# Performance work log

Hardware: AMD Instinct MI355X
Metric: run time of the kernel (lower is better)

The kernel has to match this reference:

```python
import jax, jax.numpy as jnp
import numpy as np

B, T, I, E, H = 512, 1024, 32, 32, 256  # batch, seq, input, time-enc, hidden


def setup_inputs() -> dict:
    key = jax.random.key(0)
    ks = jax.random.split(key, 10)
    s = 0.05
    return {
        "X": jax.random.normal(ks[0], (B, T, I), dtype=jnp.float32),
        "encoded_timestamps": jax.random.normal(ks[1], (B, T, E), dtype=jnp.float32),
        "mask": jax.random.randint(ks[2], (B, T), 0, 2).astype(bool),
        # GRU layer 0: input = I + E
        "w_ih0": jax.random.normal(ks[3], (3 * H, I + E), dtype=jnp.float32) * s,
        "w_hh0": jax.random.normal(ks[4], (3 * H, H), dtype=jnp.float32) * s,
        "b_ih0": jnp.zeros((3 * H,), jnp.float32),
        "b_hh0": jnp.zeros((3 * H,), jnp.float32),
        # GRU layer 1: input = H
        "w_ih1": jax.random.normal(ks[5], (3 * H, H), dtype=jnp.float32) * s,
        "w_hh1": jax.random.normal(ks[6], (3 * H, H), dtype=jnp.float32) * s,
        "b_ih1": jnp.zeros((3 * H,), jnp.float32),
        "b_hh1": jnp.zeros((3 * H,), jnp.float32),
        # readout Linear(H -> I)
        "w_out": jax.random.normal(ks[7], (I, H), dtype=jnp.float32) * s,
        "b_out": jnp.zeros((I,), jnp.float32),
    }


def _gru_cell(x, h, w_ih, w_hh, b_ih, b_hh):
    # torch GRU cell semantics (gate order r, z, n)
    gi = x @ w_ih.T + b_ih
    gh = h @ w_hh.T + b_hh
    i_r, i_z, i_n = jnp.split(gi, 3, axis=-1)
    h_r, h_z, h_n = jnp.split(gh, 3, axis=-1)
    r = jax.nn.sigmoid(i_r + h_r)
    z = jax.nn.sigmoid(i_z + h_z)
    n = jnp.tanh(i_n + r * h_n)
    return (1.0 - z) * n + z * h


def reference(X, encoded_timestamps, mask,
              w_ih0, w_hh0, b_ih0, b_hh0,
              w_ih1, w_hh1, b_ih1, b_hh1,
              w_out, b_out):
    b, t, _ = X.shape
    hdim = w_hh0.shape[1]
    tm1 = t - 1

    def step(carry, xs):
        h0, h1, y = carry
        x_t, e_t, m_t, first = xs          # x_t [B,I], e_t [B,E], m_t [B], first scalar bool
        keep = m_t | first
        inp = jnp.concatenate([jnp.where(keep[:, None], x_t, y), e_t], axis=-1)
        h0 = _gru_cell(inp, h0, w_ih0, w_hh0, b_ih0, b_hh0)
        h1 = _gru_cell(h0, h1, w_ih1, w_hh1, b_ih1, b_hh1)
        y = h1 @ w_out.T + b_out
        return (h0, h1, y), y

    init = (jnp.zeros((b, hdim), X.dtype),
            jnp.zeros((b, hdim), X.dtype),
            jnp.zeros((b, X.shape[2]), X.dtype))
    xs = (jnp.swapaxes(X[:, :tm1], 0, 1),
          jnp.swapaxes(encoded_timestamps[:, 1:], 0, 1),
          jnp.swapaxes(mask[:, :tm1], 0, 1),
          jnp.arange(tm1) == 0)
    (h0, h1, _), outs = jax.lax.scan(step, init, xs)
    output_sequence = jnp.swapaxes(outs, 0, 1)  # [B, T-1, I]
    return output_sequence, h1  # h1 == h_t[-1]
```

## Files before the change

kernel.cpp:

```cpp
#include <hip/hip_runtime.h>
#include <stdint.h>
#include <stddef.h>

typedef unsigned short u16;
typedef unsigned int u32;
typedef unsigned long long u64;
typedef __attribute__((ext_vector_type(8))) short short8;
typedef __attribute__((ext_vector_type(4))) float f32x4;
typedef __attribute__((ext_vector_type(2))) float f32x2;

#define B_    512
#define T_    1024
#define TM1_  1023
#define I_    32
#define E_    32
#define H_    256
#define GSZ   8
#define NGRP  32
#define NTH   512
#define MBOX_PAR (B_ * H_)
#define OUTY_STRIDE (TM1_ * I_)
#define OUTH_BASE ((size_t)B_ * TM1_ * I_)

__device__ __forceinline__ u16 f2bf(float f) {
  union { float f; unsigned int i; } c;
  c.f = f;
  unsigned int x = c.i;
  x += 0x7FFFu + ((x >> 16) & 1u);
  return (u16)(x >> 16);
}
__device__ __forceinline__ short8 ld8bf(const float* p) {
  short8 rv;
#pragma unroll
  for (int j = 0; j < 8; ++j) rv[j] = (short)f2bf(p[j]);
  return rv;
}
__device__ __forceinline__ float sigm(float x) { return 1.f / (1.f + __expf(-x)); }
__device__ __forceinline__ float tanh_fast(float x) {
  x = fminf(15.f, fmaxf(-15.f, x));
  float e = __expf(2.f * x);
  return (e - 1.f) / (e + 1.f);
}
__device__ __forceinline__ u64 ldq_cp(const u64* p) { return *(volatile const u64*)p; }
__device__ __forceinline__ void stw_cp(u32* p, u32 v) { *(volatile u32*)p = v; }

__global__ __launch_bounds__(NTH, 2)
void arrnn_persistent(
    const float* __restrict__ X, const float* __restrict__ ENC, const int* __restrict__ MASK,
    const float* __restrict__ wih0, const float* __restrict__ whh0,
    const float* __restrict__ bih0, const float* __restrict__ bhh0,
    const float* __restrict__ wih1, const float* __restrict__ whh1,
    const float* __restrict__ bih1, const float* __restrict__ bhh1,
    const float* __restrict__ wout, const float* __restrict__ bout,
    float* __restrict__ out, u32* __restrict__ h0m, u32* __restrict__ h1m)
{
  __shared__ __align__(16) u16 sH0buf[16 * 264];
  __shared__ __align__(16) u16 sH1buf[16 * 264];
  __shared__ __align__(16) u16 sXE[16 * 72];
  __shared__ float sGates[8 * 16 * 20];
  __shared__ float sH0loc[512];
  __shared__ float sH1loc[512];
  __shared__ float sY[16 * 36];
  __shared__ int   sMk[16];

  const int tid  = threadIdx.x;
  const int w    = tid >> 6;
  const int lane = tid & 63;
  const int quad = lane >> 4;
  const int l15  = lane & 15;
  const int g    = blockIdx.x >> 3;
  const int r    = blockIdx.x & 7;
  const int hs   = r << 5;
  const int row0 = g << 4;
  const int gt   = w >> 1;
  const int nt   = w & 1;
  const int crow = tid >> 5;
  const int c32  = tid & 31;

  short8 zero8 = {0, 0, 0, 0, 0, 0, 0, 0};

  const int gateofs = (gt == 1) ? 256 : (gt >= 2 ? 512 : 0);
  const int grow = gateofs + hs + (nt << 4) + l15;

  short8 wfA[10];
#pragma unroll
  for (int kk = 0; kk < 10; ++kk) {
    const int k = kk * 32 + quad * 8;
    const float* p;
    bool v;
    if (gt <= 1)      { v = true;     p = (k < 64) ? (wih0 + grow * 64 + k)
                                                   : (whh0 + grow * 256 + (k - 64)); }
    else if (gt == 2) { v = (kk < 2); p = wih0 + grow * 64 + (v ? k : 0); }
    else              { v = (kk < 8); p = whh0 + grow * 256 + (v ? k : 0); }
    wfA[kk] = v ? ld8bf(p) : zero8;
  }

  short8 wfB[16];
#pragma unroll
  for (int kk = 0; kk < 16; ++kk) {
    const int k = kk * 32 + quad * 8;
    const float* p;
    bool v;
    if (gt <= 1)      { v = true;     p = (k < 256) ? (wih1 + grow * 256 + k)
                                                    : (whh1 + grow * 256 + (k - 256)); }
    else if (gt == 2) { v = (kk < 8); p = wih1 + grow * 256 + (v ? k : 0); }
    else              { v = (kk < 8); p = whh1 + grow * 256 + (v ? k : 0); }
    wfB[kk] = v ? ld8bf(p) : zero8;
  }

  const int ycol = (w << 4) + l15;
  short8 wfY[8];
  if (w < 2) {
#pragma unroll
    for (int kk = 0; kk < 8; ++kk)
      wfY[kk] = ld8bf(wout + ycol * 256 + kk * 32 + quad * 8);
  } else {
#pragma unroll
    for (int kk = 0; kk < 8; ++kk) wfY[kk] = zero8;
  }
  const float boutv = (w < 2) ? bout[ycol] : 0.f;

  const int bd = hs + c32;
  const float b0r  = bih0[bd]       + bhh0[bd];
  const float b0z  = bih0[256 + bd] + bhh0[256 + bd];
  const float b0ni = bih0[512 + bd];
  const float b0nh = bhh0[512 + bd];
  const float b1r  = bih1[bd]       + bhh1[bd];
  const float b1z  = bih1[256 + bd] + bhh1[256 + bd];
  const float b1ni = bih1[512 + bd];
  const float b1nh = bhh1[512 + bd];

  for (int i = tid; i < 2112; i += NTH) {
    ((u32*)sH0buf)[i] = 0u;
    ((u32*)sH1buf)[i] = 0u;
  }
  sH0loc[tid] = 0.f;
  sH1loc[tid] = 0.f;
  __syncthreads();

  int alive = 1;
  const int b = row0 + crow;

#define SPIN_STAGE(mboxu32, expTag, dstbuf)                                      \
  do {                                                                           \
    const u64* qp = (const u64*)(mboxu32) + (size_t)b * 128 + c32 * 4;           \
    const u64 tagp = (u64)(u32)(expTag) | ((u64)(u32)(expTag) << 32);            \
    u64 q0, q1, q2, q3;                                                          \
    int it = 0;                                                                  \
    for (;;) {                                                                   \
      q0 = ldq_cp(qp); q1 = ldq_cp(qp + 1); q2 = ldq_cp(qp + 2); q3 = ldq_cp(qp + 3); \
      u64 dd = ((q0 ^ tagp) | (q1 ^ tagp) | (q2 ^ tagp) | (q3 ^ tagp))           \
               & 0x0000FFFF0000FFFFull;                                          \
      if (dd == 0 || !alive) break;                                              \
      if (++it > (1 << 16)) { alive = 0; break; }                                \
    }                                                                            \
    short8 sv;                                                                   \
    sv[0] = (short)(u16)(q0 >> 16); sv[1] = (short)(u16)(q0 >> 48);              \
    sv[2] = (short)(u16)(q1 >> 16); sv[3] = (short)(u16)(q1 >> 48);              \
    sv[4] = (short)(u16)(q2 >> 16); sv[5] = (short)(u16)(q2 >> 48);              \
    sv[6] = (short)(u16)(q3 >> 16); sv[7] = (short)(u16)(q3 >> 48);              \
    *(short8*)((dstbuf) + crow * 264 + c32 * 8) = sv;                            \
  } while (0)

  for (int t = 0; t < 1024; ++t) {
    const int par = t & 1;

    int mk = 1;
    if (t < 1023) {
      if (c32 < 16) {
        if (t > 0) mk = (MASK[b * T_ + t] != 0);
        f32x2 xld = *(const f32x2*)(X + ((size_t)b * T_ + t) * I_ + 2 * c32);
        if (mk) { sXE[crow * 72 + 2 * c32] = f2bf(xld.x);
                  sXE[crow * 72 + 2 * c32 + 1] = f2bf(xld.y); }
        if (c32 == 0) sMk[crow] = mk;
      } else {
        const int c2 = c32 - 16;
        f32x2 eld = *(const f32x2*)(ENC + ((size_t)b * T_ + t + 1) * E_ + 2 * c2);
        sXE[crow * 72 + 32 + 2 * c2] = f2bf(eld.x);
        sXE[crow * 72 + 32 + 2 * c2 + 1] = f2bf(eld.y);
      }
    }

    f32x4 accA = {0.f, 0.f, 0.f, 0.f};
    if (t < 1023) {
      const u16* ah = sH0buf + l15 * 264 + quad * 8;
      if (gt <= 1) {
#pragma unroll
        for (int kk = 2; kk < 10; ++kk)
          accA = __builtin_amdgcn_mfma_f32_16x16x32_bf16(
              *(const short8*)(ah + (kk - 2) * 32), wfA[kk], accA, 0, 0, 0);
      } else if (gt == 3) {
#pragma unroll
        for (int kk = 0; kk < 8; ++kk)
          accA = __builtin_amdgcn_mfma_f32_16x16x32_bf16(
              *(const short8*)(ah + kk * 32), wfA[kk], accA, 0, 0, 0);
      }
    }

    if (t > 0) SPIN_STAGE(h1m + (size_t)par * MBOX_PAR, t, sH1buf);
    __syncthreads();

    if (t > 0 && w < 2) {
      const u16* ap = sH1buf + l15 * 264 + quad * 8;
      f32x4 acc = {0.f, 0.f, 0.f, 0.f};
#pragma unroll
      for (int kk = 0; kk < 8; ++kk)
        acc = __builtin_amdgcn_mfma_f32_16x16x32_bf16(
            *(const short8*)(ap + kk * 32), wfY[kk], acc, 0, 0, 0);
#pragma unroll
      for (int rg = 0; rg < 4; ++rg)
        sY[(quad * 4 + rg) * 36 + ycol] = acc[rg] + boutv;
    }
    __syncthreads();

    if (t > 0) {
      if (tid < 64) {
        const int lr = (r << 1) + (tid >> 5);
        const int lc = tid & 31;
        out[(size_t)(row0 + lr) * OUTY_STRIDE + (size_t)(t - 1) * I_ + lc] =
            sY[lr * 36 + lc];
      }
      if (t < 1023 && !sMk[crow])
        sXE[crow * 72 + c32] = f2bf(sY[crow * 36 + c32]);
    }
    if (t == 1023) break;
    __syncthreads();

    if (gt <= 2) {
      const u16* axe = sXE + l15 * 72 + quad * 8;
#pragma unroll
      for (int kk = 0; kk < 2; ++kk)
        accA = __builtin_amdgcn_mfma_f32_16x16x32_bf16(
            *(const short8*)(axe + kk * 32), wfA[kk], accA, 0, 0, 0);
    }
#pragma unroll
    for (int rg = 0; rg < 4; ++rg)
      sGates[((gt << 1) | nt) * 320 + (quad * 4 + rg) * 20 + l15] = accA[rg];
    __syncthreads();

    {
      const int ntc = c32 >> 4, cc = c32 & 15;
      const float gr = sGates[((0 << 1) | ntc) * 320 + crow * 20 + cc] + b0r;
      const float gz = sGates[((1 << 1) | ntc) * 320 + crow * 20 + cc] + b0z;
      const float gi = sGates[((2 << 1) | ntc) * 320 + crow * 20 + cc] + b0ni;
      const float gh = sGates[((3 << 1) | ntc) * 320 + crow * 20 + cc] + b0nh;
      const float rr = sigm(gr);
      const float zz = sigm(gz);
      const float nn = tanh_fast(gi + rr * gh);
      const float hv = (1.f - zz) * nn + zz * sH0loc[tid];
      sH0loc[tid] = hv;
      stw_cp(h0m + (size_t)(par ^ 1) * MBOX_PAR + (size_t)b * H_ + hs + c32,
             ((u32)f2bf(hv) << 16) | (u32)(t + 1));
    }

    f32x4 accB = {0.f, 0.f, 0.f, 0.f};
    {
      const u16* a1 = sH1buf + l15 * 264 + quad * 8;
      if (gt <= 1) {
#pragma unroll
        for (int kk = 0; kk < 8; ++kk)
          accB = __builtin_amdgcn_mfma_f32_16x16x32_bf16(
              *(const short8*)(a1 + kk * 32), wfB[kk + 8], accB, 0, 0, 0);
      } else if (gt == 3) {
#pragma unroll
        for (int kk = 0; kk < 8; ++kk)
          accB = __builtin_amdgcn_mfma_f32_16x16x32_bf16(
              *(const short8*)(a1 + kk * 32), wfB[kk], accB, 0, 0, 0);
      }
    }

    SPIN_STAGE(h0m + (size_t)(par ^ 1) * MBOX_PAR, t + 1, sH0buf);
    __syncthreads();

    if (gt <= 2) {
      const u16* a0 = sH0buf + l15 * 264 + quad * 8;
#pragma unroll
      for (int kk = 0; kk < 8; ++kk)
        accB = __builtin_amdgcn_mfma_f32_16x16x32_bf16(
            *(const short8*)(a0 + kk * 32), wfB[kk], accB, 0, 0, 0);
    }
#pragma unroll
    for (int rg = 0; rg < 4; ++rg)
      sGates[((gt << 1) | nt) * 320 + (quad * 4 + rg) * 20 + l15] = accB[rg];
    __syncthreads();

    {
      const int ntc = c32 >> 4, cc = c32 & 15;
      const float gr = sGates[((0 << 1) | ntc) * 320 + crow * 20 + cc] + b1r;
      const float gz = sGates[((1 << 1) | ntc) * 320 + crow * 20 + cc] + b1z;
      const float gi = sGates[((2 << 1) | ntc) * 320 + crow * 20 + cc] + b1ni;
      const float gh = sGates[((3 << 1) | ntc) * 320 + crow * 20 + cc] + b1nh;
      const float rr = sigm(gr);
      const float zz = sigm(gz);
      const float nn = tanh_fast(gi + rr * gh);
      const float hv = (1.f - zz) * nn + zz * sH1loc[tid];
      sH1loc[tid] = hv;
      stw_cp(h1m + (size_t)(par ^ 1) * MBOX_PAR + (size_t)b * H_ + hs + c32,
             ((u32)f2bf(hv) << 16) | (u32)(t + 1));
    }
  }

  out[OUTH_BASE + (size_t)b * H_ + hs + c32] = sH1loc[tid];
#undef SPIN_STAGE
}

extern "C" void kernel_launch(void* const* d_in, const int* in_sizes, int n_in,
                              void* d_out, int out_size, void* d_ws, size_t ws_size,
                              hipStream_t stream) {
  (void)in_sizes; (void)n_in; (void)out_size; (void)ws_size;
  const float* X    = (const float*)d_in[0];
  const float* ENC  = (const float*)d_in[1];
  const int*   MASK = (const int*)d_in[2];
  const float* wih0 = (const float*)d_in[3];
  const float* whh0 = (const float*)d_in[4];
  const float* bih0 = (const float*)d_in[5];
  const float* bhh0 = (const float*)d_in[6];
  const float* wih1 = (const float*)d_in[7];
  const float* whh1 = (const float*)d_in[8];
  const float* bih1 = (const float*)d_in[9];
  const float* bhh1 = (const float*)d_in[10];
  const float* wout = (const float*)d_in[11];
  const float* bout = (const float*)d_in[12];
  float* out = (float*)d_out;

  u32* h0m = (u32*)d_ws;
  u32* h1m = h0m + 2 * (size_t)MBOX_PAR;

  hipMemsetAsync(h0m, 0, 4 * (size_t)MBOX_PAR * sizeof(u32), stream);
  arrnn_persistent<<<dim3(NGRP * GSZ), dim3(NTH), 0, stream>>>(
      X, ENC, MASK, wih0, whh0, bih0, bhh0, wih1, whh1, bih1, bhh1,
      wout, bout, out, h0m, h1m);
}
```

Measured before the change: 5.383 ms.

## Fold readout into layer-0 input weights to remove the feedback dependency stage

Precomputes the composite weights W_ih0[:, :32] @ W_out and the bias term W_ih0 @ b_out, so layer-0 gate contributions from the fed-back prediction come straight from h1 via MFMA, with no separate y computation and round-trip through shared memory. Each wave now does this h1-based product in parallel with the readout, and masked rows blend it in through a scalar factor. X, encoded timestamps and the mask are prefetched one step ahead into registers, and the x/e MFMAs move before the spin wait. This removes one barrier-separated stage from the serial critical path. In exchange there is more per-step MFMA work, more register pressure, and extra bf16 rounding from the precomposed weights.

New measurement: 9.153 ms. +70.0%, slower.

```diff
diff --git a/kernel.cpp b/kernel.cpp
--- a/kernel.cpp
+++ b/kernel.cpp
@@ -57,10 +57,9 @@
   __shared__ __align__(16) u16 sH0buf[16 * 264];
   __shared__ __align__(16) u16 sH1buf[16 * 264];
   __shared__ __align__(16) u16 sXE[16 * 72];
-  __shared__ float sGates[8 * 16 * 20];
+  __shared__ float sGates[14 * 320];
   __shared__ float sH0loc[512];
   __shared__ float sH1loc[512];
-  __shared__ float sY[16 * 36];
   __shared__ int   sMk[16];
 
   const int tid  = threadIdx.x;
@@ -108,17 +107,31 @@
     wfB[kk] = v ? ld8bf(p) : zero8;
   }
 
-  const int ycol = (w << 4) + l15;
-  short8 wfY[8];
-  if (w < 2) {
+  short8 wfG[8];
+  float boutv = 0.f;
+  if (gt == 3) {
+    const int ycol = (nt << 4) + l15;
 #pragma unroll
     for (int kk = 0; kk < 8; ++kk)
-      wfY[kk] = ld8bf(wout + ycol * 256 + kk * 32 + quad * 8);
+      wfG[kk] = ld8bf(wout + ycol * 256 + kk * 32 + quad * 8);
+    boutv = bout[ycol];
   } else {
-#pragma unroll
-    for (int kk = 0; kk < 8; ++kk) wfY[kk] = zero8;
-  }
-  const float boutv = (w < 2) ? bout[ycol] : 0.f;
+    float wrow[32];
+#pragma unroll
+    for (int j2 = 0; j2 < 32; ++j2) wrow[j2] = wih0[grow * 64 + j2];
+    for (int kk = 0; kk < 8; ++kk) {
+      short8 v8;
+#pragma unroll
+      for (int j = 0; j < 8; ++j) {
+        const int k = kk * 32 + quad * 8 + j;
+        float s = 0.f;
+#pragma unroll
+        for (int j2 = 0; j2 < 32; ++j2) s += wrow[j2] * wout[j2 * 256 + k];
+        v8[j] = (short)f2bf(s);
+      }
+      wfG[kk] = v8;
+    }
+  }
 
   const int bd = hs + c32;
   const float b0r  = bih0[bd]       + bhh0[bd];
@@ -129,6 +142,15 @@
   const float b1z  = bih1[256 + bd] + bhh1[256 + bd];
   const float b1ni = bih1[512 + bd];
   const float b1nh = bhh1[512 + bd];
+
+  float cXYr = 0.f, cXYz = 0.f, cXYn = 0.f;
+#pragma unroll
+  for (int j = 0; j < 32; ++j) {
+    const float bo = bout[j];
+    cXYr += bo * wih0[(0   + bd) * 64 + j];
+    cXYz += bo * wih0[(256 + bd) * 64 + j];
+    cXYn += bo * wih0[(512 + bd) * 64 + j];
+  }
 
   for (int i = tid; i < 2112; i += NTH) {
     ((u32*)sH0buf)[i] = 0u;
@@ -162,27 +184,37 @@
     *(short8*)((dstbuf) + crow * 264 + c32 * 8) = sv;                            \
   } while (0)
 
+  f32x2 pxe;
+  int pmk = 1;
+  if (c32 < 16) pxe = *(const f32x2*)(X + (size_t)b * T_ * I_ + 2 * c32);
+  else          pxe = *(const f32x2*)(ENC + ((size_t)b * T_ + 1) * E_ + 2 * (c32 - 16));
+
   for (int t = 0; t < 1024; ++t) {
     const int par = t & 1;
 
-    int mk = 1;
     if (t < 1023) {
       if (c32 < 16) {
-        if (t > 0) mk = (MASK[b * T_ + t] != 0);
-        f32x2 xld = *(const f32x2*)(X + ((size_t)b * T_ + t) * I_ + 2 * c32);
-        if (mk) { sXE[crow * 72 + 2 * c32] = f2bf(xld.x);
-                  sXE[crow * 72 + 2 * c32 + 1] = f2bf(xld.y); }
-        if (c32 == 0) sMk[crow] = mk;
+        const int c2 = 2 * c32;
+        sXE[crow * 72 + c2]     = pmk ? f2bf(pxe.x) : (u16)0;
+        sXE[crow * 72 + c2 + 1] = pmk ? f2bf(pxe.y) : (u16)0;
+        if (c32 == 0) sMk[crow] = pmk;
       } else {
-        const int c2 = c32 - 16;
-        f32x2 eld = *(const f32x2*)(ENC + ((size_t)b * T_ + t + 1) * E_ + 2 * c2);
-        sXE[crow * 72 + 32 + 2 * c2] = f2bf(eld.x);
-        sXE[crow * 72 + 32 + 2 * c2 + 1] = f2bf(eld.y);
-      }
-    }
+        const int c2 = 2 * (c32 - 16);
+        sXE[crow * 72 + 32 + c2]     = f2bf(pxe.x);
+        sXE[crow * 72 + 32 + c2 + 1] = f2bf(pxe.y);
+      }
+    }
+    __syncthreads();
 
     f32x4 accA = {0.f, 0.f, 0.f, 0.f};
     if (t < 1023) {
+      if (gt <= 2) {
+        const u16* axe = sXE + l15 * 72 + quad * 8;
+#pragma unroll
+        for (int kk = 0; kk < 2; ++kk)
+          accA = __builtin_amdgcn_mfma_f32_16x16x32_bf16(
+              *(const short8*)(axe + kk * 32), wfA[kk], accA, 0, 0, 0);
+      }
       const u16* ah = sH0buf + l15 * 264 + quad * 8;
       if (gt <= 1) {
 #pragma unroll
@@ -200,50 +232,47 @@
     if (t > 0) SPIN_STAGE(h1m + (size_t)par * MBOX_PAR, t, sH1buf);
     __syncthreads();
 
-    if (t > 0 && w < 2) {
-      const u16* ap = sH1buf + l15 * 264 + quad * 8;
-      f32x4 acc = {0.f, 0.f, 0.f, 0.f};
+    f32x4 accG = {0.f, 0.f, 0.f, 0.f};
+    if (t > 0 && (gt == 3 || t < 1023)) {
+      const u16* a1 = sH1buf + l15 * 264 + quad * 8;
 #pragma unroll
       for (int kk = 0; kk < 8; ++kk)
-        acc = __builtin_amdgcn_mfma_f32_16x16x32_bf16(
-            *(const short8*)(ap + kk * 32), wfY[kk], acc, 0, 0, 0);
+        accG = __builtin_amdgcn_mfma_f32_16x16x32_bf16(
+            *(const short8*)(a1 + kk * 32), wfG[kk], accG, 0, 0, 0);
+    }
+    if (t < 1023) {
 #pragma unroll
       for (int rg = 0; rg < 4; ++rg)
-        sY[(quad * 4 + rg) * 36 + ycol] = acc[rg] + boutv;
-    }
-    __syncthreads();
-
-    if (t > 0) {
-      if (tid < 64) {
-        const int lr = (r << 1) + (tid >> 5);
-        const int lc = tid & 31;
-        out[(size_t)(row0 + lr) * OUTY_STRIDE + (size_t)(t - 1) * I_ + lc] =
-            sY[lr * 36 + lc];
-      }
-      if (t < 1023 && !sMk[crow])
-        sXE[crow * 72 + c32] = f2bf(sY[crow * 36 + c32]);
+        sGates[((gt << 1) | nt) * 320 + (quad * 4 + rg) * 20 + l15] = accA[rg];
+      if (gt <= 2) {
+#pragma unroll
+        for (int rg = 0; rg < 4; ++rg)
+          sGates[(8 + ((gt << 1) | nt)) * 320 + (quad * 4 + rg) * 20 + l15] = accG[rg];
+      }
+    }
+    if (t > 0 && gt == 3) {
+#pragma unroll
+      for (int rg = 0; rg < 4; ++rg) {
+        const int row = quad * 4 + rg;
+        if ((row >> 1) == r)
+          out[(size_t)(row0 + row) * OUTY_STRIDE + (size_t)(t - 1) * I_ +
+              (nt << 4) + l15] = accG[rg] + boutv;
+      }
     }
     if (t == 1023) break;
     __syncthreads();
 
-    if (gt <= 2) {
-      const u16* axe = sXE + l15 * 72 + quad * 8;
-#pragma unroll
-      for (int kk = 0; kk < 2; ++kk)
-        accA = __builtin_amdgcn_mfma_f32_16x16x32_bf16(
-            *(const short8*)(axe + kk * 32), wfA[kk], accA, 0, 0, 0);
-    }
-#pragma unroll
-    for (int rg = 0; rg < 4; ++rg)
-      sGates[((gt << 1) | nt) * 320 + (quad * 4 + rg) * 20 + l15] = accA[rg];
-    __syncthreads();
-
     {
-      const int ntc = c32 >> 4, cc = c32 & 15;
-      const float gr = sGates[((0 << 1) | ntc) * 320 + crow * 20 + cc] + b0r;
-      const float gz = sGates[((1 << 1) | ntc) * 320 + crow * 20 + cc] + b0z;
-      const float gi = sGates[((2 << 1) | ntc) * 320 + crow * 20 + cc] + b0ni;
-      const float gh = sGates[((3 << 1) | ntc) * 320 + crow * 20 + cc] + b0nh;
+      const int ntc = c32 >> 4;
+      const int base = crow * 20 + (c32 & 15);
+      const float fm = sMk[crow] ? 0.f : 1.f;
+      const float gr = sGates[((0 << 1) | ntc) * 320 + base] +
+                       fm * (sGates[(8 + ((0 << 1) | ntc)) * 320 + base] + cXYr) + b0r;
+      const float gz = sGates[((1 << 1) | ntc) * 320 + base] +
+                       fm * (sGates[(8 + ((1 << 1) | ntc)) * 320 + base] + cXYz) + b0z;
+      const float gi = sGates[((2 << 1) | ntc) * 320 + base] +
+                       fm * (sGates[(8 + ((2 << 1) | ntc)) * 320 + base] + cXYn) + b0ni;
+      const float gh = sGates[((3 << 1) | ntc) * 320 + base] + b0nh;
       const float rr = sigm(gr);
       const float zz = sigm(gz);
       const float nn = tanh_fast(gi + rr * gh);
@@ -253,6 +282,15 @@
              ((u32)f2bf(hv) << 16) | (u32)(t + 1));
     }
 
+    if (t + 1 < 1023) {
+      if (c32 < 16) {
+        pxe = *(const f32x2*)(X + ((size_t)b * T_ + t + 1) * I_ + 2 * c32);
+        pmk = (MASK[b * T_ + t + 1] != 0);
+      } else {
+        pxe = *(const f32x2*)(ENC + ((size_t)b * T_ + t + 2) * E_ + 2 * (c32 - 16));
+      }
+    }
+
     f32x4 accB = {0.f, 0.f, 0.f, 0.f};
     {
       const u16* a1 = sH1buf + l15 * 264 + quad * 8;
@@ -285,11 +323,12 @@
     __syncthreads();
 
     {
-      const int ntc = c32 >> 4, cc = c32 & 15;
-      const float gr = sGates[((0 << 1) | ntc) * 320 + crow * 20 + cc] + b1r;
-      const float gz = sGates[((1 << 1) | ntc) * 320 + crow * 20 + cc] + b1z;
-      const float gi = sGates[((2 << 1) | ntc) * 320 + crow * 20 + cc] + b1ni;
-      const float gh = sGates[((3 << 1) | ntc) * 320 + crow * 20 + cc] + b1nh;
+      const int ntc = c32 >> 4;
+      const int base = crow * 20 + (c32 & 15);
+      const float gr = sGates[((0 << 1) | ntc) * 320 + base] + b1r;
+      const float gz = sGates[((1 << 1) | ntc) * 320 + base] + b1z;
+      const float gi = sGates[((2 << 1) | ntc) * 320 + base] + b1ni;
+      const float gh = sGates[((3 << 1) | ntc) * 320 + base] + b1nh;
       const float rr = sigm(gr);
       const float zz = sigm(gz);
       const float nn = tanh_fast(gi + rr * gh);
```
